# Kernel optimization log

Hardware: AMD Instinct MI355X
Metric: run time of the kernel (lower is better)

## Reference

```python
import jax, jax.numpy as jnp
import numpy as np

S, B, E = 3072, 1, 1024          # total tokens, batch, embed_dim
H, HK, D = 16, 8, 64              # num_heads, num_kv_heads, head_dim
SEQ_BOUNDS = [0, 1024, 2048, 3072]  # cu_seqlens: 3 images of 1024 tokens
NEG_INF = -1e9


def setup_inputs() -> dict:
    key = jax.random.key(0)
    ks = jax.random.split(key, 5)
    x = jax.random.normal(ks[0], (S, B, E), jnp.float32)
    qkv_w = jax.random.normal(ks[1], ((H + 2 * HK) * D, E), jnp.float32) * 0.02
    qkv_b = jax.random.normal(ks[2], ((H + 2 * HK) * D,), jnp.float32) * 0.02
    proj_w = jax.random.normal(ks[3], (E, H * D), jnp.float32) * 0.02
    proj_b = jax.random.normal(ks[4], (E,), jnp.float32) * 0.02
    # rotary tables: positions restart within each image window
    pos = (jnp.arange(S) % 1024).astype(jnp.float32)
    inv_freq = 1.0 / (10000.0 ** (jnp.arange(D // 2, dtype=jnp.float32) / (D // 2)))
    ang = pos[:, None] * inv_freq[None, :]            # (S, D/2)
    return {
        "x": x,
        "cu_seqlens": jnp.array(SEQ_BOUNDS, jnp.int32),
        "rotary_cos": jnp.cos(ang),
        "rotary_sin": jnp.sin(ang),
        "qkv_w": qkv_w,
        "qkv_b": qkv_b,
        "proj_w": proj_w,
        "proj_b": proj_b,
        "max_seqlen": 1024,
    }


def _apply_rope(t, cos, sin):
    # t: (b, s, h, d); cos/sin: (s, d/2) -- flash-attn non-interleaved style
    d2 = cos.shape[-1]
    t1, t2 = t[..., :d2], t[..., d2:]
    c = cos[None, :, None, :]
    s = sin[None, :, None, :]
    return jnp.concatenate([t1 * c - t2 * s, t1 * s + t2 * c], axis=-1)


def reference(x, cu_seqlens, rotary_cos, rotary_sin, qkv_w, qkv_b, proj_w, proj_b, max_seqlen):
    s_len, b = x.shape[0], x.shape[1]
    # fused QKV projection
    qkv = x @ qkv_w.T + qkv_b                          # (s, b, (H+2HK)*D)
    qkv = qkv.reshape(s_len, b, H + 2 * HK, D)
    q = jnp.transpose(qkv[:, :, :H, :], (1, 0, 2, 3))             # (b, s, H, D)
    k = jnp.transpose(qkv[:, :, H:H + HK, :], (1, 0, 2, 3))       # (b, s, HK, D)
    v = jnp.transpose(qkv[:, :, H + HK:, :], (1, 0, 2, 3))        # (b, s, HK, D)
    # rotary embedding on q and k
    q = _apply_rope(q, rotary_cos, rotary_sin)
    k = _apply_rope(k, rotary_cos, rotary_sin)
    # GQA: repeat kv heads
    k = jnp.repeat(k, H // HK, axis=2)                 # (b, s, H, D)
    v = jnp.repeat(v, H // HK, axis=2)
    # varlen (block-diagonal) attention via segment-id mask
    seg = jnp.searchsorted(cu_seqlens, jnp.arange(s_len, dtype=jnp.int32), side="right")
    mask = seg[:, None] == seg[None, :]                # (s, s)
    scale = D ** -0.5
    scores = jnp.einsum("bshd,bthd->bhst", q, k) * scale  # (b, H, s, s)
    scores = jnp.where(mask[None, None, :, :], scores, NEG_INF)
    attn = jax.nn.softmax(scores, axis=-1)
    ctx = jnp.einsum("bhst,bthd->bshd", attn, v)        # (b, s, H, D)
    # rearrange 'b s h d -> s b (h d)' and output projection
    ctx = jnp.transpose(ctx, (1, 0, 2, 3)).reshape(s_len, b, H * D)
    return ctx @ proj_w.T + proj_b                      # (s, b, E)
```

## Files before the change

### kernel.cpp

```cpp
#include <hip/hip_runtime.h>
#include <cstdint>
#include <cstddef>

#define S_LEN 3072
#define E_DIM 1024
#define NH 16
#define NKV 8
#define HD 64
#define NQKV 2048
#define SEG 1024

typedef __attribute__((ext_vector_type(8))) short bf16x8;
typedef __attribute__((ext_vector_type(4))) float f32x4;
typedef __attribute__((ext_vector_type(4))) float ff4;
typedef __attribute__((ext_vector_type(4))) short s16x4;
typedef unsigned short u16;

#define QSCALE 0.1803368801111204f

__device__ __forceinline__ u16 f2bf(float f) {
    unsigned u = __float_as_uint(f);
    u += 0x7fffu + ((u >> 16) & 1u);
    return (u16)(u >> 16);
}

__device__ __forceinline__ void gld16(const void* g, u16* l) {
    __builtin_amdgcn_global_load_lds(
        (const __attribute__((address_space(1))) unsigned*)g,
        (__attribute__((address_space(3))) unsigned*)l, 16, 0, 0);
}

__global__ __launch_bounds__(256) void k_cast(
    const float* __restrict__ x, const float* __restrict__ w, const float* __restrict__ pw,
    u16* __restrict__ xb, u16* __restrict__ wb, u16* __restrict__ pwb)
{
    const int n1 = (S_LEN * E_DIM) / 4, n2 = (NQKV * E_DIM) / 4, n3 = (E_DIM * E_DIM) / 4;
    const int total = n1 + n2 + n3;
    for (int i = blockIdx.x * 256 + threadIdx.x; i < total; i += gridDim.x * 256) {
        const float* s; u16* d; int j;
        if (i < n1)           { s = x;  d = xb;  j = i; }
        else if (i < n1 + n2) { s = w;  d = wb;  j = i - n1; }
        else                  { s = pw; d = pwb; j = i - n1 - n2; }
        ff4 v = *(const ff4*)&s[(size_t)j * 4];
        unsigned lo = (unsigned)f2bf(v.x) | ((unsigned)f2bf(v.y) << 16);
        unsigned hi = (unsigned)f2bf(v.z) | ((unsigned)f2bf(v.w) << 16);
        uint2 pk; pk.x = lo; pk.y = hi;
        *(uint2*)&d[(size_t)j * 4] = pk;
    }
}

__global__ __launch_bounds__(256) void k_qkv(
    const u16* __restrict__ xb, const u16* __restrict__ wb,
    const float* __restrict__ bias, const float* __restrict__ rc, const float* __restrict__ rs,
    u16* __restrict__ qb, u16* __restrict__ kb, u16* __restrict__ vb)
{
    __shared__ u16 smA[64 * 64];
    __shared__ u16 smB[128 * 64];
    const int tid = threadIdx.x;
    const int wv = tid >> 6, ln = tid & 63;
    const int s0 = blockIdx.x * 64;
    const int o0 = blockIdx.y * 128;
    const int wr = wv >> 1, wc = wv & 1;
    const int col = ln & 15, lg = ln >> 4;

    f32x4 acc[2][4] = {};

    for (int kt = 0; kt < E_DIM / 64; ++kt) {
        const int k0 = kt * 64;
        #pragma unroll
        for (int i = 0; i < 2; ++i) {
            int c = i * 256 + tid;
            int row = c >> 3, sl = c & 7;
            int gs = (sl ^ (row & 7)) << 3;
            gld16(&xb[(size_t)(s0 + row) * E_DIM + k0 + gs], &smA[(i * 256 + wv * 64) * 8]);
        }
        #pragma unroll
        for (int i = 0; i < 4; ++i) {
            int c = i * 256 + tid;
            int row = c >> 3, sl = c & 7;
            int gs = (sl ^ (row & 7)) << 3;
            gld16(&wb[(size_t)(o0 + row) * E_DIM + k0 + gs], &smB[(i * 256 + wv * 64) * 8]);
        }
        __syncthreads();
        #pragma unroll
        for (int ks = 0; ks < 2; ++ks) {
            bf16x8 a[2], b[4];
            #pragma unroll
            for (int mi = 0; mi < 2; ++mi) {
                int row = wr * 32 + mi * 16 + col;
                int sl = (ks * 4 + lg) ^ (row & 7);
                a[mi] = *(const bf16x8*)&smA[row * 64 + sl * 8];
            }
            #pragma unroll
            for (int ni = 0; ni < 4; ++ni) {
                int row = wc * 64 + ni * 16 + col;
                int sl = (ks * 4 + lg) ^ (row & 7);
                b[ni] = *(const bf16x8*)&smB[row * 64 + sl * 8];
            }
            #pragma unroll
            for (int mi = 0; mi < 2; ++mi)
                #pragma unroll
                for (int ni = 0; ni < 4; ++ni)
                    acc[mi][ni] = __builtin_amdgcn_mfma_f32_16x16x32_bf16(a[mi], b[ni], acc[mi][ni], 0, 0, 0);
        }
        __syncthreads();
    }

    const int ocol0 = o0 + wc * 64;
    const int head = ocol0 >> 6;
    #pragma unroll
    for (int ni = 0; ni < 4; ++ni) {
        float bv = bias[ocol0 + ni * 16 + col];
        #pragma unroll
        for (int mi = 0; mi < 2; ++mi)
            #pragma unroll
            for (int r = 0; r < 4; ++r)
                acc[mi][ni][r] += bv;
    }
    if (head < NH + NKV) {
        #pragma unroll
        for (int mi = 0; mi < 2; ++mi)
            #pragma unroll
            for (int r = 0; r < 4; ++r) {
                int s = s0 + wr * 32 + mi * 16 + lg * 4 + r;
                #pragma unroll
                for (int ni = 0; ni < 2; ++ni) {
                    int d2 = ni * 16 + col;
                    float c = rc[s * 32 + d2], sn = rs[s * 32 + d2];
                    float t1 = acc[mi][ni][r], t2 = acc[mi][ni + 2][r];
                    acc[mi][ni][r]     = t1 * c - t2 * sn;
                    acc[mi][ni + 2][r] = t1 * sn + t2 * c;
                }
            }
    }
    if (head < NH) {
        #pragma unroll
        for (int mi = 0; mi < 2; ++mi)
            #pragma unroll
            for (int ni = 0; ni < 4; ++ni)
                #pragma unroll
                for (int r = 0; r < 4; ++r)
                    acc[mi][ni][r] *= QSCALE;
    }
    if (head < NH + NKV) {
        u16* dst; int hh;
        if (head < NH) { dst = qb; hh = head; } else { dst = kb; hh = head - NH; }
        #pragma unroll
        for (int mi = 0; mi < 2; ++mi)
            #pragma unroll
            for (int r = 0; r < 4; ++r) {
                int s = s0 + wr * 32 + mi * 16 + lg * 4 + r;
                #pragma unroll
                for (int ni = 0; ni < 4; ++ni)
                    dst[((size_t)hh * S_LEN + s) * HD + ni * 16 + col] = f2bf(acc[mi][ni][r]);
            }
    } else {
        int hh = head - NH - NKV;
        #pragma unroll
        for (int mi = 0; mi < 2; ++mi) {
            int sb = s0 + wr * 32 + mi * 16 + lg * 4;
            #pragma unroll
            for (int ni = 0; ni < 4; ++ni) {
                int d = ni * 16 + col;
                s16x4 pk;
                #pragma unroll
                for (int r = 0; r < 4; ++r) pk[r] = (short)f2bf(acc[mi][ni][r]);
                *(s16x4*)&vb[((size_t)hh * HD + d) * S_LEN + sb] = pk;
            }
        }
    }
}

__global__ __launch_bounds__(256) void k_attn(
    const u16* __restrict__ qb, const u16* __restrict__ kb, const u16* __restrict__ vb,
    u16* __restrict__ cb)
{
    __shared__ u16 smK[2][64 * 64];
    __shared__ u16 smV[2][64 * 64];
    __shared__ u16 smP[4 * 16 * 64];
    const int tid = threadIdx.x;
    const int wv = tid >> 6, ln = tid & 63;
    const int h = blockIdx.y, kvh = h >> 1;
    const int s0 = blockIdx.x * 64;
    const int seg0 = s0 & ~(SEG - 1);
    const int col = ln & 15, lg = ln >> 4;

    bf16x8 qf[2];
    #pragma unroll
    for (int ks = 0; ks < 2; ++ks)
        qf[ks] = *(const bf16x8*)&qb[((size_t)h * S_LEN + s0 + wv * 16 + col) * HD + ks * 32 + lg * 8];

    f32x4 oacc[4] = {};
    float lsum[4] = {0.f, 0.f, 0.f, 0.f};
    u16* myP = &smP[wv * 16 * 64];

    const u16* Kseg = kb + ((size_t)kvh * S_LEN + seg0) * HD;
    const u16* Vseg = vb + (size_t)kvh * HD * S_LEN + seg0;

    auto stage = [&](int b, int kt) {
        #pragma unroll
        for (int i = 0; i < 2; ++i) {
            int c = i * 256 + tid; int row = c >> 3, sl = c & 7; int gs = (sl ^ (row & 7)) << 3;
            gld16(&Kseg[(size_t)(kt * 64 + row) * HD + gs], &smK[b][(i * 256 + wv * 64) * 8]);
        }
        #pragma unroll
        for (int i = 0; i < 2; ++i) {
            int c = i * 256 + tid; int row = c >> 3, sl = c & 7; int gs = (sl ^ (row & 7)) << 3;
            gld16(&Vseg[(size_t)row * S_LEN + kt * 64 + gs], &smV[b][(i * 256 + wv * 64) * 8]);
        }
    };

    stage(0, 0);
    __syncthreads();

    for (int kt = 0; kt < SEG / 64; ++kt) {
        const int cur = kt & 1;
        if (kt + 1 < SEG / 64) stage(cur ^ 1, kt + 1);

        f32x4 sacc[4] = {};
        #pragma unroll
        for (int ks = 0; ks < 2; ++ks) {
            bf16x8 kf[4];
            #pragma unroll
            for (int ni = 0; ni < 4; ++ni) {
                int row = ni * 16 + col;
                int sl = (ks * 4 + lg) ^ (row & 7);
                kf[ni] = *(const bf16x8*)&smK[cur][row * 64 + sl * 8];
            }
            #pragma unroll
            for (int ni = 0; ni < 4; ++ni)
                sacc[ni] = __builtin_amdgcn_mfma_f32_16x16x32_bf16(qf[ks], kf[ni], sacc[ni], 0, 0, 0);
        }

        #pragma unroll
        for (int ni = 0; ni < 4; ++ni)
            #pragma unroll
            for (int r = 0; r < 4; ++r) {
                float p = __builtin_amdgcn_exp2f(sacc[ni][r]);
                sacc[ni][r] = p;
                lsum[r] += p;
            }

        #pragma unroll
        for (int ni = 0; ni < 4; ++ni)
            #pragma unroll
            for (int r = 0; r < 4; ++r) {
                int row = lg * 4 + r;
                int t = ni * 16 + col;
                int b = (t >> 3) ^ (row & 7);
                myP[row * 64 + b * 8 + (t & 7)] = f2bf(sacc[ni][r]);
            }

        #pragma unroll
        for (int ks = 0; ks < 2; ++ks) {
            bf16x8 pf, vf[4];
            {
                int row = col;
                int sl = (ks * 4 + lg) ^ (row & 7);
                pf = *(const bf16x8*)&myP[row * 64 + sl * 8];
            }
            #pragma unroll
            for (int ni = 0; ni < 4; ++ni) {
                int row = ni * 16 + col;
                int sl = (ks * 4 + lg) ^ (row & 7);
                vf[ni] = *(const bf16x8*)&smV[cur][row * 64 + sl * 8];
            }
            #pragma unroll
            for (int ni = 0; ni < 4; ++ni)
                oacc[ni] = __builtin_amdgcn_mfma_f32_16x16x32_bf16(pf, vf[ni], oacc[ni], 0, 0, 0);
        }

        __syncthreads();
    }

    #pragma unroll
    for (int r = 0; r < 4; ++r) {
        float v = lsum[r];
        v += __shfl_xor(v, 1); v += __shfl_xor(v, 2);
        v += __shfl_xor(v, 4); v += __shfl_xor(v, 8);
        lsum[r] = v;
    }

    #pragma unroll
    for (int r = 0; r < 4; ++r) {
        int s = s0 + wv * 16 + lg * 4 + r;
        float inv = 1.f / lsum[r];
        #pragma unroll
        for (int ni = 0; ni < 4; ++ni) {
            int d = ni * 16 + col;
            cb[(size_t)s * E_DIM + h * HD + d] = f2bf(oacc[ni][r] * inv);
        }
    }
}

__global__ __launch_bounds__(256) void k_proj(
    const u16* __restrict__ cb, const u16* __restrict__ pwb,
    const float* __restrict__ bias, float* __restrict__ out)
{
    __shared__ u16 smA[64 * 64];
    __shared__ u16 smB[64 * 64];
    const int tid = threadIdx.x;
    const int wv = tid >> 6, ln = tid & 63;
    const int s0 = blockIdx.x * 64, o0 = blockIdx.y * 64;
    const int wr = wv >> 1, wc = wv & 1;
    const int col = ln & 15, lg = ln >> 4;

    f32x4 acc[2][2] = {};

    for (int kt = 0; kt < E_DIM / 64; ++kt) {
        const int k0 = kt * 64;
        #pragma unroll
        for (int i = 0; i < 2; ++i) {
            int c = i * 256 + tid; int row = c >> 3, sl = c & 7; int gs = (sl ^ (row & 7)) << 3;
            gld16(&cb[(size_t)(s0 + row) * E_DIM + k0 + gs], &smA[(i * 256 + wv * 64) * 8]);
        }
        #pragma unroll
        for (int i = 0; i < 2; ++i) {
            int c = i * 256 + tid; int row = c >> 3, sl = c & 7; int gs = (sl ^ (row & 7)) << 3;
            gld16(&pwb[(size_t)(o0 + row) * E_DIM + k0 + gs], &smB[(i * 256 + wv * 64) * 8]);
        }
        __syncthreads();
        #pragma unroll
        for (int ks = 0; ks < 2; ++ks) {
            bf16x8 a[2], b[2];
            #pragma unroll
            for (int mi = 0; mi < 2; ++mi) {
                int row = wr * 32 + mi * 16 + col;
                int sl = (ks * 4 + lg) ^ (row & 7);
                a[mi] = *(const bf16x8*)&smA[row * 64 + sl * 8];
            }
            #pragma unroll
            for (int ni = 0; ni < 2; ++ni) {
                int row = wc * 32 + ni * 16 + col;
                int sl = (ks * 4 + lg) ^ (row & 7);
                b[ni] = *(const bf16x8*)&smB[row * 64 + sl * 8];
            }
            #pragma unroll
            for (int mi = 0; mi < 2; ++mi)
                #pragma unroll
                for (int ni = 0; ni < 2; ++ni)
                    acc[mi][ni] = __builtin_amdgcn_mfma_f32_16x16x32_bf16(a[mi], b[ni], acc[mi][ni], 0, 0, 0);
        }
        __syncthreads();
    }

    #pragma unroll
    for (int mi = 0; mi < 2; ++mi)
        #pragma unroll
        for (int r = 0; r < 4; ++r) {
            int s = s0 + wr * 32 + mi * 16 + lg * 4 + r;
            #pragma unroll
            for (int ni = 0; ni < 2; ++ni) {
                int o = o0 + wc * 32 + ni * 16 + col;
                out[(size_t)s * E_DIM + o] = acc[mi][ni][r] + bias[o];
            }
        }
}

extern "C" void kernel_launch(void* const* d_in, const int* in_sizes, int n_in,
                              void* d_out, int out_size, void* d_ws, size_t ws_size,
                              hipStream_t stream) {
    const float* x      = (const float*)d_in[0];
    const float* rc     = (const float*)d_in[2];
    const float* rs     = (const float*)d_in[3];
    const float* qkv_w  = (const float*)d_in[4];
    const float* qkv_b  = (const float*)d_in[5];
    const float* proj_w = (const float*)d_in[6];
    const float* proj_b = (const float*)d_in[7];
    float* out = (float*)d_out;

    u16* ws  = (u16*)d_ws;
    u16* xb  = ws;
    u16* wb  = xb  + (size_t)S_LEN * E_DIM;
    u16* pwb = wb  + (size_t)NQKV * E_DIM;
    u16* qb  = pwb + (size_t)E_DIM * E_DIM;
    u16* kb  = qb  + (size_t)NH * S_LEN * HD;
    u16* vb  = kb  + (size_t)NKV * S_LEN * HD;
    u16* cb  = vb  + (size_t)NKV * S_LEN * HD;

    k_cast<<<1536, 256, 0, stream>>>(x, qkv_w, proj_w, xb, wb, pwb);
    k_qkv <<<dim3(48, 16), 256, 0, stream>>>(xb, wb, qkv_b, rc, rs, qb, kb, vb);
    k_attn<<<dim3(48, 16), 256, 0, stream>>>(qb, kb, vb, cb);
    k_proj<<<dim3(48, 16), 256, 0, stream>>>(cb, pwb, proj_b, out);
}
```

Before: 143.7 us.

## Double-buffer LDS tiles in QKV and output projection GEMMs

Both the QKV projection and the output projection kernels now keep two shared-memory buffers per operand. While the current K tile is consumed by MFMAs, the direct global-to-LDS loads for the next tile are issued. The aim is to overlap global load latency with compute and cut a barrier per iteration. LDS use doubles, which may lower occupancy, and the gld16 completion wait still relies on the existing end-of-iteration barrier.

```diff
diff --git a/kernel.cpp b/kernel.cpp
--- a/kernel.cpp
+++ b/kernel.cpp
@@ -54,8 +54,8 @@
     const float* __restrict__ bias, const float* __restrict__ rc, const float* __restrict__ rs,
     u16* __restrict__ qb, u16* __restrict__ kb, u16* __restrict__ vb)
 {
-    __shared__ u16 smA[64 * 64];
-    __shared__ u16 smB[128 * 64];
+    __shared__ u16 smA[2][64 * 64];
+    __shared__ u16 smB[2][128 * 64];
     const int tid = threadIdx.x;
     const int wv = tid >> 6, ln = tid & 63;
     const int s0 = blockIdx.x * 64;
@@ -65,23 +65,30 @@
 
     f32x4 acc[2][4] = {};
 
-    for (int kt = 0; kt < E_DIM / 64; ++kt) {
+    auto stage = [&](int b, int kt) {
         const int k0 = kt * 64;
         #pragma unroll
         for (int i = 0; i < 2; ++i) {
             int c = i * 256 + tid;
             int row = c >> 3, sl = c & 7;
             int gs = (sl ^ (row & 7)) << 3;
-            gld16(&xb[(size_t)(s0 + row) * E_DIM + k0 + gs], &smA[(i * 256 + wv * 64) * 8]);
+            gld16(&xb[(size_t)(s0 + row) * E_DIM + k0 + gs], &smA[b][(i * 256 + wv * 64) * 8]);
         }
         #pragma unroll
         for (int i = 0; i < 4; ++i) {
             int c = i * 256 + tid;
             int row = c >> 3, sl = c & 7;
             int gs = (sl ^ (row & 7)) << 3;
-            gld16(&wb[(size_t)(o0 + row) * E_DIM + k0 + gs], &smB[(i * 256 + wv * 64) * 8]);
-        }
-        __syncthreads();
+            gld16(&wb[(size_t)(o0 + row) * E_DIM + k0 + gs], &smB[b][(i * 256 + wv * 64) * 8]);
+        }
+    };
+
+    stage(0, 0);
+    __syncthreads();
+
+    for (int kt = 0; kt < E_DIM / 64; ++kt) {
+        const int cur = kt & 1;
+        if (kt + 1 < E_DIM / 64) stage(cur ^ 1, kt + 1);
         #pragma unroll
         for (int ks = 0; ks < 2; ++ks) {
             bf16x8 a[2], b[4];
@@ -89,13 +96,13 @@
             for (int mi = 0; mi < 2; ++mi) {
                 int row = wr * 32 + mi * 16 + col;
                 int sl = (ks * 4 + lg) ^ (row & 7);
-                a[mi] = *(const bf16x8*)&smA[row * 64 + sl * 8];
+                a[mi] = *(const bf16x8*)&smA[cur][row * 64 + sl * 8];
             }
             #pragma unroll
             for (int ni = 0; ni < 4; ++ni) {
                 int row = wc * 64 + ni * 16 + col;
                 int sl = (ks * 4 + lg) ^ (row & 7);
-                b[ni] = *(const bf16x8*)&smB[row * 64 + sl * 8];
+                b[ni] = *(const bf16x8*)&smB[cur][row * 64 + sl * 8];
             }
             #pragma unroll
             for (int mi = 0; mi < 2; ++mi)
@@ -297,8 +304,8 @@
     const u16* __restrict__ cb, const u16* __restrict__ pwb,
     const float* __restrict__ bias, float* __restrict__ out)
 {
-    __shared__ u16 smA[64 * 64];
-    __shared__ u16 smB[64 * 64];
+    __shared__ u16 smA[2][64 * 64];
+    __shared__ u16 smB[2][64 * 64];
     const int tid = threadIdx.x;
     const int wv = tid >> 6, ln = tid & 63;
     const int s0 = blockIdx.x * 64, o0 = blockIdx.y * 64;
@@ -307,19 +314,26 @@
 
     f32x4 acc[2][2] = {};
 
+    auto stage = [&](int b, int kt) {
+        const int k0 = kt * 64;
+        #pragma unroll
+        for (int i = 0; i < 2; ++i) {
+            int c = i * 256 + tid; int row = c >> 3, sl = c & 7; int gs = (sl ^ (row & 7)) << 3;
+            gld16(&cb[(size_t)(s0 + row) * E_DIM + k0 + gs], &smA[b][(i * 256 + wv * 64) * 8]);
+        }
+        #pragma unroll
+        for (int i = 0; i < 2; ++i) {
+            int c = i * 256 + tid; int row = c >> 3, sl = c & 7; int gs = (sl ^ (row & 7)) << 3;
+            gld16(&pwb[(size_t)(o0 + row) * E_DIM + k0 + gs], &smB[b][(i * 256 + wv * 64) * 8]);
+        }
+    };
+
+    stage(0, 0);
+    __syncthreads();
+
     for (int kt = 0; kt < E_DIM / 64; ++kt) {
-        const int k0 = kt * 64;
-        #pragma unroll
-        for (int i = 0; i < 2; ++i) {
-            int c = i * 256 + tid; int row = c >> 3, sl = c & 7; int gs = (sl ^ (row & 7)) << 3;
-            gld16(&cb[(size_t)(s0 + row) * E_DIM + k0 + gs], &smA[(i * 256 + wv * 64) * 8]);
-        }
-        #pragma unroll
-        for (int i = 0; i < 2; ++i) {
-            int c = i * 256 + tid; int row = c >> 3, sl = c & 7; int gs = (sl ^ (row & 7)) << 3;
-            gld16(&pwb[(size_t)(o0 + row) * E_DIM + k0 + gs], &smB[(i * 256 + wv * 64) * 8]);
-        }
-        __syncthreads();
+        const int cur = kt & 1;
+        if (kt + 1 < E_DIM / 64) stage(cur ^ 1, kt + 1);
         #pragma unroll
         for (int ks = 0; ks < 2; ++ks) {
             bf16x8 a[2], b[2];
@@ -327,13 +341,13 @@
             for (int mi = 0; mi < 2; ++mi) {
                 int row = wr * 32 + mi * 16 + col;
                 int sl = (ks * 4 + lg) ^ (row & 7);
-                a[mi] = *(const bf16x8*)&smA[row * 64 + sl * 8];
+                a[mi] = *(const bf16x8*)&smA[cur][row * 64 + sl * 8];
             }
             #pragma unroll
             for (int ni = 0; ni < 2; ++ni) {
                 int row = wc * 32 + ni * 16 + col;
                 int sl = (ks * 4 + lg) ^ (row & 7);
-                b[ni] = *(const bf16x8*)&smB[row * 64 + sl * 8];
+                b[ni] = *(const bf16x8*)&smB[cur][row * 64 + sl * 8];
             }
             #pragma unroll
             for (int mi = 0; mi < 2; ++mi)
```

New measurement: 147.6 us. 1.03x slower.

## Keep attention probabilities in registers by computing S transposed and using 16x16x16 MFMA

Applied to the files above, without the earlier changes.

The attention kernel now computes the score tile as K·Q^T, so each lane's accumulator already holds the layout the PV MFMA wants as its A operand. The probabilities are packed to bf16 with v_cvt_pk_bf16_f32 and fed straight into mfma_16x16x16bf16_1k, which removes the per-wave shared-memory P buffer and its store/load round trip. The row-sum reduction becomes cross-lane shuffles followed by a broadcast. The trade-off is twice as many smaller MFMAs for PV and narrower 8-byte LDS reads of V. The old path is kept behind a builtin-availability check.

```diff
diff --git a/kernel.cpp b/kernel.cpp
--- a/kernel.cpp
+++ b/kernel.cpp
@@ -11,12 +11,18 @@
 #define SEG 1024
 
 typedef __attribute__((ext_vector_type(8))) short bf16x8;
+typedef __attribute__((ext_vector_type(4))) short s16x4;
 typedef __attribute__((ext_vector_type(4))) float f32x4;
 typedef __attribute__((ext_vector_type(4))) float ff4;
-typedef __attribute__((ext_vector_type(4))) short s16x4;
 typedef unsigned short u16;
 
 #define QSCALE 0.1803368801111204f
+
+#if defined(__has_builtin)
+#if __has_builtin(__builtin_amdgcn_mfma_f32_16x16x16bf16_1k)
+#define HAVE_MFMA16 1
+#endif
+#endif
 
 __device__ __forceinline__ u16 f2bf(float f) {
     unsigned u = __float_as_uint(f);
@@ -177,7 +183,9 @@
 {
     __shared__ u16 smK[2][64 * 64];
     __shared__ u16 smV[2][64 * 64];
+#ifndef HAVE_MFMA16
     __shared__ u16 smP[4 * 16 * 64];
+#endif
     const int tid = threadIdx.x;
     const int wv = tid >> 6, ln = tid & 63;
     const int h = blockIdx.y, kvh = h >> 1;
@@ -191,8 +199,6 @@
         qf[ks] = *(const bf16x8*)&qb[((size_t)h * S_LEN + s0 + wv * 16 + col) * HD + ks * 32 + lg * 8];
 
     f32x4 oacc[4] = {};
-    float lsum[4] = {0.f, 0.f, 0.f, 0.f};
-    u16* myP = &smP[wv * 16 * 64];
 
     const u16* Kseg = kb + ((size_t)kvh * S_LEN + seg0) * HD;
     const u16* Vseg = vb + (size_t)kvh * HD * S_LEN + seg0;
@@ -213,6 +219,9 @@
     stage(0, 0);
     __syncthreads();
 
+#ifdef HAVE_MFMA16
+    float lsum = 0.f;
+
     for (int kt = 0; kt < SEG / 64; ++kt) {
         const int cur = kt & 1;
         if (kt + 1 < SEG / 64) stage(cur ^ 1, kt + 1);
@@ -229,18 +238,82 @@
             }
             #pragma unroll
             for (int ni = 0; ni < 4; ++ni)
+                sacc[ni] = __builtin_amdgcn_mfma_f32_16x16x32_bf16(kf[ni], qf[ks], sacc[ni], 0, 0, 0);
+        }
+
+        s16x4 pk4[4];
+        #pragma unroll
+        for (int ni = 0; ni < 4; ++ni) {
+            float p0 = __builtin_amdgcn_exp2f(sacc[ni][0]);
+            float p1 = __builtin_amdgcn_exp2f(sacc[ni][1]);
+            float p2 = __builtin_amdgcn_exp2f(sacc[ni][2]);
+            float p3 = __builtin_amdgcn_exp2f(sacc[ni][3]);
+            lsum += (p0 + p1) + (p2 + p3);
+            unsigned lo, hi;
+            asm("v_cvt_pk_bf16_f32 %0, %1, %2" : "=v"(lo) : "v"(p0), "v"(p1));
+            asm("v_cvt_pk_bf16_f32 %0, %1, %2" : "=v"(hi) : "v"(p2), "v"(p3));
+            union { unsigned u[2]; s16x4 v; } pu;
+            pu.u[0] = lo; pu.u[1] = hi;
+            pk4[ni] = pu.v;
+        }
+
+        #pragma unroll
+        for (int nk = 0; nk < 4; ++nk) {
+            #pragma unroll
+            for (int nd = 0; nd < 4; ++nd) {
+                int row = nd * 16 + col;
+                int sl = (2 * nk + (lg >> 1)) ^ (row & 7);
+                s16x4 vf4 = *(const s16x4*)&smV[cur][row * 64 + sl * 8 + (lg & 1) * 4];
+                oacc[nd] = __builtin_amdgcn_mfma_f32_16x16x16bf16_1k(pk4[nk], vf4, oacc[nd], 0, 0, 0);
+            }
+        }
+
+        __syncthreads();
+    }
+
+    lsum += __shfl_xor(lsum, 16);
+    lsum += __shfl_xor(lsum, 32);
+
+    #pragma unroll
+    for (int r = 0; r < 4; ++r) {
+        float ls = __shfl(lsum, lg * 4 + r);
+        int s = s0 + wv * 16 + lg * 4 + r;
+        float inv = 1.f / ls;
+        #pragma unroll
+        for (int nd = 0; nd < 4; ++nd)
+            cb[(size_t)s * E_DIM + h * HD + nd * 16 + col] = f2bf(oacc[nd][r] * inv);
+    }
+
+#else
+    float lsum4[4] = {0.f, 0.f, 0.f, 0.f};
+    u16* myP = &smP[wv * 16 * 64];
+
+    for (int kt = 0; kt < SEG / 64; ++kt) {
+        const int cur = kt & 1;
+        if (kt + 1 < SEG / 64) stage(cur ^ 1, kt + 1);
+
+        f32x4 sacc[4] = {};
+        #pragma unroll
+        for (int ks = 0; ks < 2; ++ks) {
+            bf16x8 kf[4];
+            #pragma unroll
+            for (int ni = 0; ni < 4; ++ni) {
+                int row = ni * 16 + col;
+                int sl = (ks * 4 + lg) ^ (row & 7);
+                kf[ni] = *(const bf16x8*)&smK[cur][row * 64 + sl * 8];
+            }
+            #pragma unroll
+            for (int ni = 0; ni < 4; ++ni)
                 sacc[ni] = __builtin_amdgcn_mfma_f32_16x16x32_bf16(qf[ks], kf[ni], sacc[ni], 0, 0, 0);
         }
-
         #pragma unroll
         for (int ni = 0; ni < 4; ++ni)
             #pragma unroll
             for (int r = 0; r < 4; ++r) {
                 float p = __builtin_amdgcn_exp2f(sacc[ni][r]);
                 sacc[ni][r] = p;
-                lsum[r] += p;
-            }
-
+                lsum4[r] += p;
+            }
         #pragma unroll
         for (int ni = 0; ni < 4; ++ni)
             #pragma unroll
@@ -250,7 +323,6 @@
                 int b = (t >> 3) ^ (row & 7);
                 myP[row * 64 + b * 8 + (t & 7)] = f2bf(sacc[ni][r]);
             }
-
         #pragma unroll
         for (int ks = 0; ks < 2; ++ks) {
             bf16x8 pf, vf[4];
@@ -269,28 +341,25 @@
             for (int ni = 0; ni < 4; ++ni)
                 oacc[ni] = __builtin_amdgcn_mfma_f32_16x16x32_bf16(pf, vf[ni], oacc[ni], 0, 0, 0);
         }
-
         __syncthreads();
     }
 
     #pragma unroll
     for (int r = 0; r < 4; ++r) {
-        float v = lsum[r];
+        float v = lsum4[r];
         v += __shfl_xor(v, 1); v += __shfl_xor(v, 2);
         v += __shfl_xor(v, 4); v += __shfl_xor(v, 8);
-        lsum[r] = v;
-    }
-
+        lsum4[r] = v;
+    }
     #pragma unroll
     for (int r = 0; r < 4; ++r) {
         int s = s0 + wv * 16 + lg * 4 + r;
-        float inv = 1.f / lsum[r];
-        #pragma unroll
-        for (int ni = 0; ni < 4; ++ni) {
-            int d = ni * 16 + col;
-            cb[(size_t)s * E_DIM + h * HD + d] = f2bf(oacc[ni][r] * inv);
-        }
-    }
+        float inv = 1.f / lsum4[r];
+        #pragma unroll
+        for (int ni = 0; ni < 4; ++ni)
+            cb[(size_t)s * E_DIM + h * HD + ni * 16 + col] = f2bf(oacc[ni][r] * inv);
+    }
+#endif
 }
 
 __global__ __launch_bounds__(256) void k_proj(
```

Measured after the change: 142.1 us. No clear change (-1.1%).
